# Optimization experiments

Measured on AMD Instinct MI355X. Metric: run time of the kernel, lower is better.

Reference implementation:

```python
import jax, jax.numpy as jnp
import numpy as np

B, N, K = 4, 4096, 16
DP, DM = 64, 128
EPS = 1e-8


def setup_inputs() -> dict:
    key = jax.random.key(0)
    ks = jax.random.split(key, 32)
    g = lambda i, shape, fan: jax.random.normal(ks[i], shape, jnp.float32) / np.sqrt(fan)
    inp = {
        'xyz': jax.random.normal(ks[0], (B, N, 3), jnp.float32),
        'features': jax.random.normal(ks[1], (B, N, DP), jnp.float32),
        # fc1: d_points -> d_model
        'fc1_w': g(2, (DP, DM), DP), 'fc1_b': jnp.zeros((DM,), jnp.float32),
        # fc2: d_model -> d_points
        'fc2_w': g(3, (DM, DP), DM), 'fc2_b': jnp.zeros((DP,), jnp.float32),
        # fc_delta: Linear(3,DM) -> ReLU -> Linear(DM,DM)
        'd1_w': g(4, (3, DM), 3), 'd1_b': jnp.zeros((DM,), jnp.float32),
        'd2_w': g(5, (DM, DM), DM), 'd2_b': jnp.zeros((DM,), jnp.float32),
        # fc_gamma: Linear(DM,DM) -> ReLU -> Linear(DM,DM)
        'g1_w': g(6, (DM, DM), DM), 'g1_b': jnp.zeros((DM,), jnp.float32),
        'g2_w': g(7, (DM, DM), DM), 'g2_b': jnp.zeros((DM,), jnp.float32),
        # q/k/v projections, no bias
        'wq_w': g(8, (DM, DM), DM), 'wk_w': g(9, (DM, DM), DM), 'wv_w': g(10, (DM, DM), DM),
        # fc_sim: Linear(DM+1, DM)
        'sim_w': g(11, (DM + 1, DM), DM + 1), 'sim_b': jnp.zeros((DM,), jnp.float32),
    }
    return inp


def _gather(t, idx):
    # t: [B, N, C], idx: [B, N, K] -> [B, N, K, C]
    bidx = jnp.arange(t.shape[0])[:, None, None]
    return t[bidx, idx]


def reference(xyz, features, fc1_w, fc1_b, fc2_w, fc2_b, d1_w, d1_b, d2_w, d2_b,
              g1_w, g1_b, g2_w, g2_b, wq_w, wk_w, wv_w, sim_w, sim_b):
    # pairwise squared distances [B, N, N]
    sq = jnp.sum(xyz * xyz, axis=-1)
    dists = sq[:, :, None] + sq[:, None, :] - 2.0 * jnp.einsum('bnc,bmc->bnm', xyz, xyz)
    knn_idx = jnp.argsort(dists, axis=-1)[:, :, :K]            # [B, N, K]

    knn_xyz = _gather(xyz, knn_idx)                            # [B, N, K, 3]
    x = features @ fc1_w + fc1_b                               # [B, N, DM]
    q = x @ wq_w                                               # [B, N, DM]
    k = _gather(x @ wk_w, knn_idx)                             # [B, N, K, DM]
    v = _gather(x @ wv_w, knn_idx)                             # [B, N, K, DM]

    rel_pos = xyz[:, :, None, :] - knn_xyz                     # [B, N, K, 3]
    pos_enc = jax.nn.relu(rel_pos @ d1_w + d1_b) @ d2_w + d2_b # [B, N, K, DM]

    qe = q[:, :, None, :]                                      # [B, N, 1, DM]
    # torch cosine_similarity: dot / (max(||q||,eps) * max(||k||,eps))
    qn = jnp.maximum(jnp.linalg.norm(q, axis=-1), EPS)[:, :, None]
    kn = jnp.maximum(jnp.linalg.norm(k, axis=-1), EPS)
    sim = jnp.sum(qe * k, axis=-1) / (qn * kn)                 # [B, N, K]

    rel_qk = jnp.concatenate([sim[..., None], qe - k], axis=-1)  # [B, N, K, DM+1]
    rel_qk = rel_qk @ sim_w + sim_b                            # [B, N, K, DM]

    attn = jax.nn.relu((rel_qk + pos_enc) @ g1_w + g1_b) @ g2_w + g2_b
    attn = jax.nn.softmax(attn / np.sqrt(DM).astype(np.float32), axis=-2)  # over K

    res = jnp.einsum('bnkf,bnkf->bnf', attn, v + pos_enc)      # [B, N, DM]
    res = res @ fc2_w + fc2_b + features                       # [B, N, DP]
    return res, attn
```

## Files before the change

### kernel.cpp

```cpp
#include <hip/hip_runtime.h>
#include <hip/hip_bf16.h>

#define BB 4
#define NN 4096
#define KK 16
#define DP 64
#define DM 128
#define DMP 132
#define SPITCH 264
#define EPSF 1e-8f
#define OUT0N ((size_t)BB * NN * DP)

typedef unsigned short u16t;
typedef __attribute__((ext_vector_type(8))) short s8v;
typedef __attribute__((ext_vector_type(4))) float f4v;

__device__ int g_flag;

__device__ __forceinline__ float u2f(u16t u) {
    unsigned int x = ((unsigned int)u) << 16;
    return __uint_as_float(x);
}
__device__ __forceinline__ u16t f2u(float v) {
    __hip_bfloat16 h = __float2bfloat16(v);
    return *(u16t*)&h;
}
__device__ __forceinline__ void splitf(float x, u16t& h, u16t& l) {
    const unsigned xb = __float_as_uint(x);
    h = (u16t)(xb >> 16);
    const float hf = __uint_as_float(xb & 0xffff0000u);
    l = (u16t)(__float_as_uint(x - hf) >> 16);
}

template<int DT> struct IO;
template<> struct IO<0> {
    static __device__ __forceinline__ float ld(const void* p, size_t i) { return ((const float*)p)[i]; }
    static __device__ __forceinline__ void ld4(const void* p, size_t i, float o[4]) {
        float4 v = *(const float4*)((const float*)p + i);
        o[0] = v.x; o[1] = v.y; o[2] = v.z; o[3] = v.w;
    }
    static __device__ __forceinline__ void st(void* p, size_t i, float v) { ((float*)p)[i] = v; }
};
template<> struct IO<1> {
    static __device__ __forceinline__ float ld(const void* p, size_t i) { return u2f(((const u16t*)p)[i]); }
    static __device__ __forceinline__ void ld4(const void* p, size_t i, float o[4]) {
        ushort4 v = *(const ushort4*)((const u16t*)p + i);
        o[0] = u2f(v.x); o[1] = u2f(v.y); o[2] = u2f(v.z); o[3] = u2f(v.w);
    }
    static __device__ __forceinline__ void st(void* p, size_t i, float v) { ((u16t*)p)[i] = f2u(v); }
};

__global__ __launch_bounds__(64) void detect_kernel(const void* feat) {
    const int tid = threadIdx.x;
    float x = u2f(((const u16t*)feat)[2 * tid]);
    float a = fabsf(x);
    bool sane = (x == 0.0f) || (a > 1e-4f && a < 50.0f);
    unsigned long long m = __ballot(sane);
    if (tid == 0) g_flag = (__popcll(m) >= 32) ? 1 : 0;
}

struct QkvSmem { float sf[DP]; float sx[DM]; };

template<int DT>
__device__ __forceinline__ void qkv_body(QkvSmem& s,
    const void* feat, const void* fc1_w, const void* fc1_b,
    const void* wq, const void* wk, const void* wv,
    float* __restrict__ qbuf, float* __restrict__ kbuf, float* __restrict__ vbuf)
{
    const int bn = blockIdx.x;
    const int tid = threadIdx.x;
    if (tid < DP) s.sf[tid] = IO<DT>::ld(feat, (size_t)bn * DP + tid);
    __syncthreads();
    float x = IO<DT>::ld(fc1_b, tid);
#pragma unroll 4
    for (int i = 0; i < DP; i++) x = fmaf(s.sf[i], IO<DT>::ld(fc1_w, i * DM + tid), x);
    s.sx[tid] = x;
    __syncthreads();
    float q = 0.f, k = 0.f, v = 0.f;
    for (int i0 = 0; i0 < DM; i0 += 4) {
        float4 xv = *(const float4*)&s.sx[i0];
        const float xs[4] = { xv.x, xv.y, xv.z, xv.w };
#pragma unroll
        for (int j = 0; j < 4; j++) {
            q = fmaf(xs[j], IO<DT>::ld(wq, (i0 + j) * DM + tid), q);
            k = fmaf(xs[j], IO<DT>::ld(wk, (i0 + j) * DM + tid), k);
            v = fmaf(xs[j], IO<DT>::ld(wv, (i0 + j) * DM + tid), v);
        }
    }
    qbuf[(size_t)bn * DM + tid] = q;
    kbuf[(size_t)bn * DM + tid] = k;
    vbuf[(size_t)bn * DM + tid] = v;
}

__global__ __launch_bounds__(128) void qkv_kernel(
    const void* feat, const void* fc1_w, const void* fc1_b,
    const void* wq, const void* wk, const void* wv,
    float* qbuf, float* kbuf, float* vbuf)
{
    __shared__ __align__(16) QkvSmem s;
    if (g_flag) qkv_body<1>(s, feat, fc1_w, fc1_b, wq, wk, wv, qbuf, kbuf, vbuf);
    else        qkv_body<0>(s, feat, fc1_w, fc1_b, wq, wk, wv, qbuf, kbuf, vbuf);
}

struct Qkv16Smem { float sf[16][DP]; float sx[16][DMP]; };

template<int DT>
__device__ __forceinline__ void qkv16_body(Qkv16Smem& s,
    const void* feat, const void* fc1_w, const void* fc1_b,
    const void* wq, const void* wk, const void* wv,
    float* __restrict__ qbuf, float* __restrict__ kbuf, float* __restrict__ vbuf)
{
    const int pnt0 = blockIdx.x << 4;
    const int tid = threadIdx.x;
    {
        const int r = tid >> 4, c4 = (tid & 15) << 2;
        float o[4];
        IO<DT>::ld4(feat, (size_t)(pnt0 + r) * DP + c4, o);
        s.sf[r][c4 + 0] = o[0]; s.sf[r][c4 + 1] = o[1];
        s.sf[r][c4 + 2] = o[2]; s.sf[r][c4 + 3] = o[3];
    }
    __syncthreads();
    const int c = tid & 127, h = tid >> 7;
    {
        float acc[8];
        const float fb = IO<DT>::ld(fc1_b, c);
#pragma unroll
        for (int pp = 0; pp < 8; pp++) acc[pp] = fb;
        for (int i = 0; i < DP; i++) {
            const float w = IO<DT>::ld(fc1_w, (size_t)i * DM + c);
#pragma unroll
            for (int pp = 0; pp < 8; pp++) acc[pp] = fmaf(s.sf[h * 8 + pp][i], w, acc[pp]);
        }
#pragma unroll
        for (int pp = 0; pp < 8; pp++) s.sx[h * 8 + pp][c] = acc[pp];
    }
    __syncthreads();
    {
        float aq[8], ak[8], av[8];
#pragma unroll
        for (int pp = 0; pp < 8; pp++) { aq[pp] = 0.f; ak[pp] = 0.f; av[pp] = 0.f; }
        for (int i0 = 0; i0 < DM; i0 += 4) {
            float x4[8][4];
#pragma unroll
            for (int pp = 0; pp < 8; pp++) {
                const float4 xv = *(const float4*)&s.sx[h * 8 + pp][i0];
                x4[pp][0] = xv.x; x4[pp][1] = xv.y; x4[pp][2] = xv.z; x4[pp][3] = xv.w;
            }
#pragma unroll
            for (int j = 0; j < 4; j++) {
                const float wqv = IO<DT>::ld(wq, (size_t)(i0 + j) * DM + c);
                const float wkv = IO<DT>::ld(wk, (size_t)(i0 + j) * DM + c);
                const float wvv = IO<DT>::ld(wv, (size_t)(i0 + j) * DM + c);
#pragma unroll
                for (int pp = 0; pp < 8; pp++) {
                    aq[pp] = fmaf(x4[pp][j], wqv, aq[pp]);
                    ak[pp] = fmaf(x4[pp][j], wkv, ak[pp]);
                    av[pp] = fmaf(x4[pp][j], wvv, av[pp]);
                }
            }
        }
#pragma unroll
        for (int pp = 0; pp < 8; pp++) {
            const size_t row = (size_t)(pnt0 + h * 8 + pp) * DM + c;
            qbuf[row] = aq[pp]; kbuf[row] = ak[pp]; vbuf[row] = av[pp];
        }
    }
}

__global__ __launch_bounds__(256) void qkv16_kernel(
    const void* feat, const void* fc1_w, const void* fc1_b,
    const void* wq, const void* wk, const void* wv,
    float* qbuf, float* kbuf, float* vbuf)
{
    __shared__ __align__(16) Qkv16Smem s;
    if (g_flag) qkv16_body<1>(s, feat, fc1_w, fc1_b, wq, wk, wv, qbuf, kbuf, vbuf);
    else        qkv16_body<0>(s, feat, fc1_w, fc1_b, wq, wk, wv, qbuf, kbuf, vbuf);
}

template<int DT>
__device__ __forceinline__ void knn_body(float4* __restrict__ sc,
    const void* xyz, int* dst, int dstride, void* dout, int in_out)
{
    if (in_out) {
        if (DT) { dst = (int*)((u16t*)dout + OUT0N); dstride = (KK * DM) / 2; }
        else    { dst = (int*)((float*)dout + OUT0N); dstride = KK * DM; }
    }
    const int b = blockIdx.x >> 9;
    const int tid = threadIdx.x;
    for (int j = tid; j < NN; j += 512) {
        float x = IO<DT>::ld(xyz, ((size_t)b * NN + j) * 3 + 0);
        float y = IO<DT>::ld(xyz, ((size_t)b * NN + j) * 3 + 1);
        float z = IO<DT>::ld(xyz, ((size_t)b * NN + j) * 3 + 2);
        float sq = __fadd_rn(__fadd_rn(__fmul_rn(x, x), __fmul_rn(y, y)), __fmul_rn(z, z));
        sc[j] = make_float4(x, y, z, sq);
    }
    __syncthreads();
    const int lane = tid & 63;
    const int wave = tid >> 6;
    const int r = ((blockIdx.x & 511) << 3) + wave;
    const float4 qc = sc[r];

    float d[KK];
    int id[KK];
#pragma unroll
    for (int t = 0; t < KK; t++) { d[t] = 3.4e38f; id[t] = 0x7fffffff; }

    for (int j = lane; j < NN; j += 64) {
        const float4 c = sc[j];
        const float dot = __fadd_rn(__fadd_rn(__fmul_rn(qc.x, c.x), __fmul_rn(qc.y, c.y)),
                                    __fmul_rn(qc.z, c.z));
        const float dist = __fsub_rn(__fadd_rn(qc.w, c.w), __fmul_rn(2.0f, dot));
        if (dist < d[KK - 1]) {
            float cd = dist; int ci = j;
#pragma unroll
            for (int t = 0; t < KK; t++) {
                const bool sw = (cd < d[t]);
                const float od = d[t]; const int oi = id[t];
                d[t]  = sw ? cd : d[t];
                id[t] = sw ? ci : id[t];
                cd = sw ? od : cd;
                ci = sw ? oi : ci;
            }
        }
    }

    const size_t base = (size_t)(b * NN + r) * (size_t)dstride;
#pragma unroll
    for (int t = 0; t < KK; t++) {
        float bd = d[0]; int bi = id[0];
#pragma unroll
        for (int off = 32; off >= 1; off >>= 1) {
            const float od = __shfl_xor(bd, off, 64);
            const int   oi = __shfl_xor(bi, off, 64);
            if (od < bd || (od == bd && oi < bi)) { bd = od; bi = oi; }
        }
        const bool win = (d[0] == bd) && (id[0] == bi);
        if (win) {
#pragma unroll
            for (int u = 0; u < KK - 1; u++) { d[u] = d[u + 1]; id[u] = id[u + 1]; }
            d[KK - 1] = 3.4e38f; id[KK - 1] = 0x7fffffff;
        }
        if (lane == t) dst[base + t] = bi;
    }
}

__global__ __launch_bounds__(512) void knn_kernel(
    const void* xyz, int* dst, int dstride, void* dout, int in_out)
{
    __shared__ __align__(16) float4 sc[NN];
    if (g_flag) knn_body<1>(sc, xyz, dst, dstride, dout, in_out);
    else        knn_body<0>(sc, xyz, dst, dstride, dout, in_out);
}

template<int DT>
__device__ __forceinline__ void gemm_tile(const float* __restrict__ IN,
                                          const void* __restrict__ W, int woff,
                                          int kg, int f0, float acc[4][4])
{
#pragma unroll
    for (int a = 0; a < 4; a++)
#pragma unroll
        for (int c = 0; c < 4; c++) acc[a][c] = 0.f;
    for (int i0 = 0; i0 < DM; i0 += 4) {
        float w[4][4];
#pragma unroll
        for (int j = 0; j < 4; j++) IO<DT>::ld4(W, (size_t)woff + (i0 + j) * DM + f0, w[j]);
#pragma unroll
        for (int kk = 0; kk < 4; kk++) {
            float4 x4 = *(const float4*)(IN + (kg * 4 + kk) * DMP + i0);
            const float xs[4] = { x4.x, x4.y, x4.z, x4.w };
#pragma unroll
            for (int ff = 0; ff < 4; ff++)
#pragma unroll
                for (int j = 0; j < 4; j++)
                    acc[kk][ff] = fmaf(xs[j], w[j][ff], acc[kk][ff]);
        }
    }
}

template<int DT>
__device__ __forceinline__ void wprep_body(const void* sim_w, const void* d2_w,
                                           const void* g1_w, const void* g2_w,
                                           u16t* __restrict__ wprep)
{
    const int m  = blockIdx.x >> 3;
    const int t  = blockIdx.x & 7;
    const int ks = threadIdx.x >> 6;
    const int lane = threadIdx.x & 63;
    const void* src = (m == 0) ? sim_w : (m == 1) ? d2_w : (m == 2) ? g1_w : g2_w;
    const int srcoff = (m == 0) ? DM : 0;
    u16t* hi = wprep + (size_t)m * 32768;
    u16t* lo = hi + 16384;
    const int c  = t * 16 + (lane & 15);
    const int k0 = ks * 32 + ((lane >> 4) << 3);
    s8v vh, vl;
#pragma unroll
    for (int j = 0; j < 8; j++) {
        const float x = IO<DT>::ld(src, (size_t)srcoff + (size_t)(k0 + j) * DM + c);
        const u16t h = f2u(x);
        vh[j] = (short)h;
        vl[j] = (short)f2u(x - u2f(h));
    }
    const size_t off = ((size_t)(t * 4 + ks) * 64 + lane) * 8;
    *(s8v*)(hi + off) = vh;
    *(s8v*)(lo + off) = vl;
}

__global__ __launch_bounds__(256) void wprep_kernel(
    const void* sim_w, const void* d2_w, const void* g1_w, const void* g2_w,
    u16t* wprep)
{
    if (g_flag) wprep_body<1>(sim_w, d2_w, g1_w, g2_w, wprep);
    else        wprep_body<0>(sim_w, d2_w, g1_w, g2_w, wprep);
}

__device__ __forceinline__ void mfma_core(const u16t* __restrict__ SP,
                                          const u16t* __restrict__ wmat,
                                          int lane, int wid, f4v acc[4])
{
    const u16t* whi = wmat;
    const u16t* wlo = wmat + 16384;
    const u16t* ar = SP + (size_t)(lane & 15) * SPITCH + ((lane >> 4) << 3);
#pragma unroll
    for (int ks = 0; ks < 4; ks++) {
        const s8v ahi = *(const s8v*)(ar + ks * 32);
        const s8v alo = *(const s8v*)(ar + 128 + ks * 32);
#pragma unroll
        for (int t = 0; t < 4; t++) {
            const size_t off = ((size_t)((wid * 4 + t) * 4 + ks) * 64 + lane) * 8;
            const s8v bhi = *(const s8v*)(whi + off);
            const s8v blo = *(const s8v*)(wlo + off);
            acc[t] = __builtin_amdgcn_mfma_f32_16x16x32_bf16(ahi, bhi, acc[t], 0, 0, 0);
            acc[t] = __builtin_amdgcn_mfma_f32_16x16x32_bf16(ahi, blo, acc[t], 0, 0, 0);
            acc[t] = __builtin_amdgcn_mfma_f32_16x16x32_bf16(alo, bhi, acc[t], 0, 0, 0);
        }
    }
}

struct AttnSmemS {
    float KF[KK * DMP];
    float T1[KK * DMP];
    u16t  SP[KK * SPITCH];
    float s_q[DM];
    float sred[DM];
    float sp2[DM];
    float srp[KK][3];
    float ssim[KK];
    int   sidx[KK];
};

template<int DT>
__device__ __forceinline__ void attn_sp_body(AttnSmemS& s,
    const void* xyz, const void* feat,
    const void* fc2_w, const void* fc2_b,
    const void* d1_w, const void* d1_b, const void* d2_b,
    const void* g1_b, const void* g2_b,
    const void* sim_w, const void* sim_b,
    const float* __restrict__ qbuf, const float* __restrict__ kbuf,
    const float* __restrict__ vbuf,
    const int* __restrict__ knn, const u16t* __restrict__ wprep, void* dout)
{
    void* out0 = dout;
    void* out1 = DT ? (void*)((u16t*)dout + OUT0N) : (void*)((float*)dout + OUT0N);
    const int bn = blockIdx.x;
    const int b = bn >> 12;
    const int tid = threadIdx.x;
    const int f = tid;
    const int lane = tid & 63;
    const int wid = tid >> 6;

    if (tid < KK) {
        int sv = knn[(size_t)bn * KK + tid];
        sv = (sv < 0) ? 0 : (sv > NN - 1 ? NN - 1 : sv);
        s.sidx[tid] = sv;
    }
    __syncthreads();

    float vreg[KK];
    {
        s.s_q[f] = qbuf[(size_t)bn * DM + f];
#pragma unroll
        for (int k = 0; k < KK; k++) {
            const int grow = (b << 12) + s.sidx[k];
            s.KF[k * DMP + f] = kbuf[(size_t)grow * DM + f];
            vreg[k] = vbuf[(size_t)grow * DM + f];
        }
    }
    if (tid < KK) {
        const int grow = (b << 12) + s.sidx[tid];
#pragma unroll
        for (int c = 0; c < 3; c++)
            s.srp[tid][c] = IO<DT>::ld(xyz, (size_t)bn * 3 + c) - IO<DT>::ld(xyz, (size_t)grow * 3 + c);
    }
    __syncthreads();

    {
        const int j = tid >> 3, g = tid & 7;
        float sk = 0.f, sd = 0.f, qq = 0.f;
#pragma unroll
        for (int i4 = 0; i4 < 16; i4 += 4) {
            const float4 kv = *(const float4*)&s.KF[j * DMP + g * 16 + i4];
            const float4 qv = *(const float4*)&s.s_q[g * 16 + i4];
            sk = fmaf(kv.x, kv.x, fmaf(kv.y, kv.y, fmaf(kv.z, kv.z, fmaf(kv.w, kv.w, sk))));
            sd = fmaf(qv.x, kv.x, fmaf(qv.y, kv.y, fmaf(qv.z, kv.z, fmaf(qv.w, kv.w, sd))));
            qq = fmaf(qv.x, qv.x, fmaf(qv.y, qv.y, fmaf(qv.z, qv.z, fmaf(qv.w, qv.w, qq))));
        }
#pragma unroll
        for (int off = 1; off <= 4; off <<= 1) {
            sk += __shfl_xor(sk, off, 64);
            sd += __shfl_xor(sd, off, 64);
            qq += __shfl_xor(qq, off, 64);
        }
        if (g == 0) {
            const float qn = fmaxf(sqrtf(qq), EPSF);
            const float kn = fmaxf(sqrtf(sk), EPSF);
            s.ssim[j] = sd / (qn * kn);
        }
    }
    {
        const int r = tid & 15, c0 = (tid >> 4) << 4;
        u16t* hp = &s.SP[r * SPITCH + c0];
        u16t* lp = hp + 128;
#pragma unroll
        for (int j4 = 0; j4 < 16; j4 += 4) {
            const float4 kv = *(const float4*)&s.KF[r * DMP + c0 + j4];
            const float4 qv = *(const float4*)&s.s_q[c0 + j4];
            ushort4 hv, lv;
            splitf(qv.x - kv.x, hv.x, lv.x);
            splitf(qv.y - kv.y, hv.y, lv.y);
            splitf(qv.z - kv.z, hv.z, lv.z);
            splitf(qv.w - kv.w, hv.w, lv.w);
            *(ushort4*)(hp + j4) = hv;
            *(ushort4*)(lp + j4) = lv;
        }
    }
    __syncthreads();

    {
        f4v acc[4] = { {0,0,0,0},{0,0,0,0},{0,0,0,0},{0,0,0,0} };
        mfma_core(s.SP, wprep + 0 * 32768, lane, wid, acc);
        const int r0 = (lane >> 4) * 4;
#pragma unroll
        for (int t = 0; t < 4; t++) {
            const int col = (wid * 4 + t) * 16 + (lane & 15);
            const float bv = IO<DT>::ld(sim_b, col);
            const float w0v = IO<DT>::ld(sim_w, col);
#pragma unroll
            for (int r = 0; r < 4; r++)
                s.T1[(size_t)(r0 + r) * DMP + col] = fmaf(s.ssim[r0 + r], w0v, acc[t][r] + bv);
        }
    }
    __syncthreads();

    {
        const int r = tid & 15, c0 = (tid >> 4) << 4;
        const float rx = s.srp[r][0], ry = s.srp[r][1], rz = s.srp[r][2];
        u16t* hp = &s.SP[r * SPITCH + c0];
        u16t* lp = hp + 128;
#pragma unroll
        for (int j4 = 0; j4 < 16; j4 += 4) {
            float w0[4], w1[4], w2[4], bb[4];
            IO<DT>::ld4(d1_w, (size_t)0 * DM + c0 + j4, w0);
            IO<DT>::ld4(d1_w, (size_t)1 * DM + c0 + j4, w1);
            IO<DT>::ld4(d1_w, (size_t)2 * DM + c0 + j4, w2);
            IO<DT>::ld4(d1_b, c0 + j4, bb);
            ushort4 hv, lv;
#pragma unroll
            for (int jj = 0; jj < 4; jj++) {
                const float h = fmaxf(fmaf(rz, w2[jj], fmaf(ry, w1[jj], fmaf(rx, w0[jj], bb[jj]))), 0.f);
                u16t hs, ls; splitf(h, hs, ls);
                ((u16t*)&hv)[jj] = hs; ((u16t*)&lv)[jj] = ls;
            }
            *(ushort4*)(hp + j4) = hv;
            *(ushort4*)(lp + j4) = lv;
        }
    }
    __syncthreads();

    {
        f4v acc[4] = { {0,0,0,0},{0,0,0,0},{0,0,0,0},{0,0,0,0} };
        mfma_core(s.SP, wprep + 1 * 32768, lane, wid, acc);
        const int r0 = (lane >> 4) * 4;
#pragma unroll
        for (int t = 0; t < 4; t++) {
            const int col = (wid * 4 + t) * 16 + (lane & 15);
            const float bv = IO<DT>::ld(d2_b, col);
#pragma unroll
            for (int r = 0; r < 4; r++)
                s.KF[(size_t)(r0 + r) * DMP + col] = acc[t][r] + bv;
        }
    }
    __syncthreads();

    {
        const int r = tid & 15, c0 = (tid >> 4) << 4;
        u16t* hp = &s.SP[r * SPITCH + c0];
        u16t* lp = hp + 128;
#pragma unroll
        for (int j4 = 0; j4 < 16; j4 += 4) {
            const float4 t4 = *(const float4*)&s.T1[r * DMP + c0 + j4];
            const float4 p4 = *(const float4*)&s.KF[r * DMP + c0 + j4];
            ushort4 hv, lv;
            splitf(t4.x + p4.x, hv.x, lv.x);
            splitf(t4.y + p4.y, hv.y, lv.y);
            splitf(t4.z + p4.z, hv.z, lv.z);
            splitf(t4.w + p4.w, hv.w, lv.w);
            *(ushort4*)(hp + j4) = hv;
            *(ushort4*)(lp + j4) = lv;
        }
    }
    __syncthreads();

    {
        f4v acc[4] = { {0,0,0,0},{0,0,0,0},{0,0,0,0},{0,0,0,0} };
        mfma_core(s.SP, wprep + 2 * 32768, lane, wid, acc);
        __syncthreads();
        const int r0 = (lane >> 4) * 4;
#pragma unroll
        for (int t = 0; t < 4; t++) {
            const int col = (wid * 4 + t) * 16 + (lane & 15);
            const float bv = IO<DT>::ld(g1_b, col);
#pragma unroll
            for (int r = 0; r < 4; r++) {
                const float v = fmaxf(acc[t][r] + bv, 0.f);
                u16t hs, ls; splitf(v, hs, ls);
                s.SP[(size_t)(r0 + r) * SPITCH + col] = hs;
                s.SP[(size_t)(r0 + r) * SPITCH + 128 + col] = ls;
            }
        }
    }
    __syncthreads();

    {
        f4v acc[4] = { {0,0,0,0},{0,0,0,0},{0,0,0,0},{0,0,0,0} };
        mfma_core(s.SP, wprep + 3 * 32768, lane, wid, acc);
        const int r0 = (lane >> 4) * 4;
#pragma unroll
        for (int t = 0; t < 4; t++) {
            const int col = (wid * 4 + t) * 16 + (lane & 15);
            const float bv = IO<DT>::ld(g2_b, col);
#pragma unroll
            for (int r = 0; r < 4; r++)
                s.T1[(size_t)(r0 + r) * DMP + col] = acc[t][r] + bv;
        }
    }
    __syncthreads();

    {
        const float inv = 0.08838834764831843f;
        float tv[KK];
        float mx = -3.4e38f;
#pragma unroll
        for (int k = 0; k < KK; k++) { tv[k] = s.T1[k * DMP + f] * inv; mx = fmaxf(mx, tv[k]); }
        float ssum = 0.f;
#pragma unroll
        for (int k = 0; k < KK; k++) { tv[k] = __expf(tv[k] - mx); ssum += tv[k]; }
        const float rs = 1.0f / ssum;
        float rf = 0.f;
#pragma unroll
        for (int k = 0; k < KK; k++) {
            const float a = tv[k] * rs;
            IO<DT>::st(out1, ((size_t)bn * KK + k) * DM + f, a);
            rf = fmaf(a, vreg[k] + s.KF[k * DMP + f], rf);
        }
        s.sred[f] = rf;
    }
    __syncthreads();

    {
        const int c = tid & 63, hh = tid >> 6;
        float o = 0.f;
        for (int i = hh * 64; i < hh * 64 + 64; i++)
            o = fmaf(s.sred[i], IO<DT>::ld(fc2_w, (size_t)i * DP + c), o);
        s.sp2[tid] = o;
    }
    __syncthreads();
    if (tid < DP) {
        float o = s.sp2[tid] + s.sp2[tid + 64];
        o = o + IO<DT>::ld(fc2_b, tid) + IO<DT>::ld(feat, (size_t)bn * DP + tid);
        IO<DT>::st(out0, (size_t)bn * DP + tid, o);
    }
}

__global__ __launch_bounds__(128) void attn_sp_kernel(
    const void* xyz, const void* feat,
    const void* fc2_w, const void* fc2_b,
    const void* d1_w, const void* d1_b, const void* d2_b,
    const void* g1_b, const void* g2_b,
    const void* sim_w, const void* sim_b,
    const float* qbuf, const float* kbuf, const float* vbuf,
    const int* knn, const u16t* wprep, void* dout)
{
    __shared__ __align__(16) AttnSmemS s;
    if (g_flag)
        attn_sp_body<1>(s, xyz, feat, fc2_w, fc2_b, d1_w, d1_b, d2_b, g1_b, g2_b,
                        sim_w, sim_b, qbuf, kbuf, vbuf, knn, wprep, dout);
    else
        attn_sp_body<0>(s, xyz, feat, fc2_w, fc2_b, d1_w, d1_b, d2_b, g1_b, g2_b,
                        sim_w, sim_b, qbuf, kbuf, vbuf, knn, wprep, dout);
}

template<bool FUSED> struct AttnSmem {
    float Kb[KK * DMP], Vb[KK * DMP], PE[KK * DMP], T0[KK * DMP], T1[KK * DMP];
    float s_q[DM], sres[DM];
    float SF[FUSED ? 17 * DP : 1];
    float X[FUSED ? 17 * DMP : 1];
    float srp[KK][3];
    float ssim[KK], skn[KK], sdot[KK];
    float sqn;
    int sidx[KK];
};

template<int DT, bool FUSED>
__device__ __forceinline__ void attn_body(AttnSmem<FUSED>& s,
    const void* xyz, const void* feat,
    const void* fc1_w, const void* fc1_b, const void* fc2_w, const void* fc2_b,
    const void* d1_w, const void* d1_b, const void* d2_w, const void* d2_b,
    const void* g1_w, const void* g1_b, const void* g2_w, const void* g2_b,
    const void* sim_w, const void* sim_b,
    const void* wq, const void* wk, const void* wv,
    const float* __restrict__ qbuf, const float* __restrict__ kbuf, const float* __restrict__ vbuf,
    const int* knn, int knn_stride, int knn_in_out, void* dout)
{
    void* out0 = dout;
    void* out1 = DT ? (void*)((u16t*)dout + OUT0N) : (void*)((float*)dout + OUT0N);
    if (knn_in_out) {
        if (DT) { knn = (const int*)((const u16t*)dout + OUT0N); knn_stride = (KK * DM) / 2; }
        else    { knn = (const int*)((const float*)dout + OUT0N); knn_stride = KK * DM; }
    }

    const int bn = blockIdx.x;
    const int b = bn >> 12;
    const int tid = threadIdx.x;
    const int f = tid;
    const int f0 = (tid & 31) * 4;
    const int kg = tid >> 5;

    if (tid < KK) {
        int sv = knn[(size_t)bn * knn_stride + tid];
        sv = (sv < 0) ? 0 : (sv > NN - 1 ? NN - 1 : sv);
        s.sidx[tid] = sv;
    }
    __syncthreads();

    if constexpr (FUSED) {
        for (int idx = tid; idx < 17 * DP; idx += 128) {
            const int r = idx >> 6, c = idx & 63;
            const int row = (r < KK) ? ((b << 12) + s.sidx[r]) : bn;
            s.SF[idx] = IO<DT>::ld(feat, (size_t)row * DP + c);
        }
        __syncthreads();
        float xacc[17];
        const float fb = IO<DT>::ld(fc1_b, tid);
#pragma unroll
        for (int r = 0; r < 17; r++) xacc[r] = fb;
        for (int i = 0; i < DP; i++) {
            const float w = IO<DT>::ld(fc1_w, i * DM + tid);
#pragma unroll
            for (int r = 0; r < 17; r++) xacc[r] = fmaf(s.SF[r * DP + i], w, xacc[r]);
        }
#pragma unroll
        for (int r = 0; r < 17; r++) s.X[r * DMP + tid] = xacc[r];
        __syncthreads();
        {
            float a2[4][4];
            gemm_tile<DT>(s.X, wk, 0, kg, f0, a2);
#pragma unroll
            for (int kk = 0; kk < 4; kk++)
                *(float4*)&s.Kb[(kg * 4 + kk) * DMP + f0] =
                    make_float4(a2[kk][0], a2[kk][1], a2[kk][2], a2[kk][3]);
            gemm_tile<DT>(s.X, wv, 0, kg, f0, a2);
#pragma unroll
            for (int kk = 0; kk < 4; kk++)
                *(float4*)&s.Vb[(kg * 4 + kk) * DMP + f0] =
                    make_float4(a2[kk][0], a2[kk][1], a2[kk][2], a2[kk][3]);
        }
        {
            float qv = 0.f;
            for (int i0 = 0; i0 < DM; i0 += 4) {
                float4 x4 = *(const float4*)&s.X[16 * DMP + i0];
                const float xs[4] = { x4.x, x4.y, x4.z, x4.w };
#pragma unroll
                for (int j = 0; j < 4; j++)
                    qv = fmaf(xs[j], IO<DT>::ld(wq, (i0 + j) * DM + tid), qv);
            }
            s.s_q[tid] = qv;
        }
    } else {
        s.s_q[f] = qbuf[(size_t)bn * DM + f];
#pragma unroll
        for (int k = 0; k < KK; k++) {
            const int row = (b << 12) + s.sidx[k];
            s.Kb[k * DMP + f] = kbuf[(size_t)row * DM + f];
            s.Vb[k * DMP + f] = vbuf[(size_t)row * DM + f];
        }
    }
    if (tid < KK) {
        const int row = (b << 12) + s.sidx[tid];
#pragma unroll
        for (int c = 0; c < 3; c++)
            s.srp[tid][c] = IO<DT>::ld(xyz, (size_t)bn * 3 + c) - IO<DT>::ld(xyz, (size_t)row * 3 + c);
    }
    __syncthreads();

    if (tid < KK) {
        float sk = 0.f, sd = 0.f;
        for (int i = 0; i < DM; i++) {
            float v2 = s.Kb[tid * DMP + i];
            sk = fmaf(v2, v2, sk);
            sd = fmaf(s.s_q[i], v2, sd);
        }
        s.skn[tid] = fmaxf(sqrtf(sk), EPSF);
        s.sdot[tid] = sd;
    } else if (tid == KK) {
        float sqq = 0.f;
        for (int i = 0; i < DM; i++) { float v2 = s.s_q[i]; sqq = fmaf(v2, v2, sqq); }
        s.sqn = fmaxf(sqrtf(sqq), EPSF);
    }
    __syncthreads();
    if (tid < KK) s.ssim[tid] = s.sdot[tid] / (s.sqn * s.skn[tid]);
#pragma unroll
    for (int k = 0; k < KK; k++) s.T0[k * DMP + f] = s.s_q[f] - s.Kb[k * DMP + f];
    __syncthreads();

    float acc[4][4];

    gemm_tile<DT>(s.T0, sim_w, DM, kg, f0, acc);
    {
        float w0f[4], sbf[4];
        IO<DT>::ld4(sim_w, f0, w0f);
        IO<DT>::ld4(sim_b, f0, sbf);
#pragma unroll
        for (int kk = 0; kk < 4; kk++) {
            float sm = s.ssim[kg * 4 + kk];
            float4 o;
            o.x = fmaf(sm, w0f[0], acc[kk][0]) + sbf[0];
            o.y = fmaf(sm, w0f[1], acc[kk][1]) + sbf[1];
            o.z = fmaf(sm, w0f[2], acc[kk][2]) + sbf[2];
            o.w = fmaf(sm, w0f[3], acc[kk][3]) + sbf[3];
            *(float4*)&s.T1[(kg * 4 + kk) * DMP + f0] = o;
        }
    }
    __syncthreads();

    {
        float w0 = IO<DT>::ld(d1_w, 0 * DM + f), w1 = IO<DT>::ld(d1_w, 1 * DM + f),
              w2 = IO<DT>::ld(d1_w, 2 * DM + f);
        float hb = IO<DT>::ld(d1_b, f);
#pragma unroll
        for (int k = 0; k < KK; k++) {
            float h = fmaf(s.srp[k][2], w2, fmaf(s.srp[k][1], w1, fmaf(s.srp[k][0], w0, hb)));
            s.T0[k * DMP + f] = fmaxf(h, 0.f);
        }
    }
    __syncthreads();

    gemm_tile<DT>(s.T0, d2_w, 0, kg, f0, acc);
    {
        float bf[4];
        IO<DT>::ld4(d2_b, f0, bf);
#pragma unroll
        for (int kk = 0; kk < 4; kk++)
            *(float4*)&s.PE[(kg * 4 + kk) * DMP + f0] =
                make_float4(acc[kk][0] + bf[0], acc[kk][1] + bf[1],
                            acc[kk][2] + bf[2], acc[kk][3] + bf[3]);
    }
    __syncthreads();

#pragma unroll
    for (int kk = 0; kk < 4; kk++) {
        const int row = (kg * 4 + kk) * DMP + f0;
        float4 a4 = *(const float4*)&s.T1[row];
        float4 p4 = *(const float4*)&s.PE[row];
        *(float4*)&s.T0[row] = make_float4(a4.x + p4.x, a4.y + p4.y, a4.z + p4.z, a4.w + p4.w);
    }
    __syncthreads();

    gemm_tile<DT>(s.T0, g1_w, 0, kg, f0, acc);
    {
        float bf[4];
        IO<DT>::ld4(g1_b, f0, bf);
#pragma unroll
        for (int kk = 0; kk < 4; kk++)
            *(float4*)&s.T1[(kg * 4 + kk) * DMP + f0] =
                make_float4(fmaxf(acc[kk][0] + bf[0], 0.f), fmaxf(acc[kk][1] + bf[1], 0.f),
                            fmaxf(acc[kk][2] + bf[2], 0.f), fmaxf(acc[kk][3] + bf[3], 0.f));
    }
    __syncthreads();

    gemm_tile<DT>(s.T1, g2_w, 0, kg, f0, acc);
    {
        float bf[4];
        IO<DT>::ld4(g2_b, f0, bf);
#pragma unroll
        for (int kk = 0; kk < 4; kk++)
            *(float4*)&s.T0[(kg * 4 + kk) * DMP + f0] =
                make_float4(acc[kk][0] + bf[0], acc[kk][1] + bf[1],
                            acc[kk][2] + bf[2], acc[kk][3] + bf[3]);
    }
    __syncthreads();

    {
        const float sq128 = 11.31370849898476f;
        float tv[KK];
        float m = -3.4e38f;
#pragma unroll
        for (int k = 0; k < KK; k++) { tv[k] = s.T0[k * DMP + f] / sq128; m = fmaxf(m, tv[k]); }
        float ssum = 0.f;
#pragma unroll
        for (int k = 0; k < KK; k++) { tv[k] = expf(tv[k] - m); ssum += tv[k]; }
        float rf = 0.f;
#pragma unroll
        for (int k = 0; k < KK; k++) {
            float a = tv[k] / ssum;
            IO<DT>::st(out1, ((size_t)bn * KK + k) * DM + f, a);
            rf = fmaf(a, s.Vb[k * DMP + f] + s.PE[k * DMP + f], rf);
        }
        s.sres[f] = rf;
    }
    __syncthreads();

    if (tid < DP) {
        float o = 0.f;
        for (int i = 0; i < DM; i++) o = fmaf(s.sres[i], IO<DT>::ld(fc2_w, i * DP + tid), o);
        o = o + IO<DT>::ld(fc2_b, tid) + IO<DT>::ld(feat, (size_t)bn * DP + tid);
        IO<DT>::st(out0, (size_t)bn * DP + tid, o);
    }
}

template<bool FUSED>
__global__ __launch_bounds__(128) void attn_kernel(
    const void* xyz, const void* feat,
    const void* fc1_w, const void* fc1_b, const void* fc2_w, const void* fc2_b,
    const void* d1_w, const void* d1_b, const void* d2_w, const void* d2_b,
    const void* g1_w, const void* g1_b, const void* g2_w, const void* g2_b,
    const void* sim_w, const void* sim_b,
    const void* wq, const void* wk, const void* wv,
    const float* qbuf, const float* kbuf, const float* vbuf,
    const int* knn, int knn_stride, int knn_in_out, void* dout)
{
    __shared__ __align__(16) AttnSmem<FUSED> s;
    if (g_flag)
        attn_body<1, FUSED>(s, xyz, feat, fc1_w, fc1_b, fc2_w, fc2_b, d1_w, d1_b, d2_w, d2_b,
                            g1_w, g1_b, g2_w, g2_b, sim_w, sim_b, wq, wk, wv,
                            qbuf, kbuf, vbuf, knn, knn_stride, knn_in_out, dout);
    else
        attn_body<0, FUSED>(s, xyz, feat, fc1_w, fc1_b, fc2_w, fc2_b, d1_w, d1_b, d2_w, d2_b,
                            g1_w, g1_b, g2_w, g2_b, sim_w, sim_b, wq, wk, wv,
                            qbuf, kbuf, vbuf, knn, knn_stride, knn_in_out, dout);
}

extern "C" void kernel_launch(void* const* d_in, const int* in_sizes, int n_in,
                              void* d_out, int out_size, void* d_ws, size_t ws_size,
                              hipStream_t stream)
{
    const void* xyz   = d_in[0];
    const void* feat  = d_in[1];
    const void* fc1_w = d_in[2];
    const void* fc1_b = d_in[3];
    const void* fc2_w = d_in[4];
    const void* fc2_b = d_in[5];
    const void* d1_w  = d_in[6];
    const void* d1_b  = d_in[7];
    const void* d2_w  = d_in[8];
    const void* d2_b  = d_in[9];
    const void* g1_w  = d_in[10];
    const void* g1_b  = d_in[11];
    const void* g2_w  = d_in[12];
    const void* g2_b  = d_in[13];
    const void* wq_w  = d_in[14];
    const void* wk_w  = d_in[15];
    const void* wv_w  = d_in[16];
    const void* sim_w = d_in[17];
    const void* sim_b = d_in[18];

    detect_kernel<<<1, 64, 0, stream>>>(feat);

    const size_t need_qkv = (size_t)3 * BB * NN * DM * sizeof(float);
    const size_t need_knn = (size_t)BB * NN * KK * sizeof(int);
    const size_t need_wp  = (size_t)4 * 2 * 16384 * sizeof(u16t);

    if (ws_size >= need_qkv + need_knn + need_wp && d_ws != nullptr) {
        float* qbuf  = (float*)d_ws;
        float* kbuf  = qbuf + (size_t)BB * NN * DM;
        float* vbuf  = kbuf + (size_t)BB * NN * DM;
        int*   knn   = (int*)(vbuf + (size_t)BB * NN * DM);
        u16t*  wprep = (u16t*)(knn + (size_t)BB * NN * KK);
        qkv16_kernel<<<(BB * NN) / 16, 256, 0, stream>>>(feat, fc1_w, fc1_b, wq_w, wk_w, wv_w,
                                                         qbuf, kbuf, vbuf);
        knn_kernel<<<BB * 512, 512, 0, stream>>>(xyz, knn, KK, d_out, 0);
        wprep_kernel<<<32, 256, 0, stream>>>(sim_w, d2_w, g1_w, g2_w, wprep);
        attn_sp_kernel<<<BB * NN, 128, 0, stream>>>(
            xyz, feat, fc2_w, fc2_b, d1_w, d1_b, d2_b, g1_b, g2_b, sim_w, sim_b,
            qbuf, kbuf, vbuf, knn, wprep, d_out);
    } else if (ws_size >= need_qkv + need_knn && d_ws != nullptr) {
        float* qbuf = (float*)d_ws;
        float* kbuf = qbuf + (size_t)BB * NN * DM;
        float* vbuf = kbuf + (size_t)BB * NN * DM;
        int*   knn  = (int*)(vbuf + (size_t)BB * NN * DM);
        qkv_kernel<<<BB * NN, DM, 0, stream>>>(feat, fc1_w, fc1_b, wq_w, wk_w, wv_w, qbuf, kbuf, vbuf);
        knn_kernel<<<BB * 512, 512, 0, stream>>>(xyz, knn, KK, d_out, 0);
        attn_kernel<false><<<BB * NN, DM, 0, stream>>>(
            xyz, feat, fc1_w, fc1_b, fc2_w, fc2_b, d1_w, d1_b, d2_w, d2_b,
            g1_w, g1_b, g2_w, g2_b, sim_w, sim_b, wq_w, wk_w, wv_w,
            qbuf, kbuf, vbuf, knn, KK, 0, d_out);
    } else if (ws_size >= need_knn && d_ws != nullptr) {
        int* knn = (int*)d_ws;
        knn_kernel<<<BB * 512, 512, 0, stream>>>(xyz, knn, KK, d_out, 0);
        attn_kernel<true><<<BB * NN, DM, 0, stream>>>(
            xyz, feat, fc1_w, fc1_b, fc2_w, fc2_b, d1_w, d1_b, d2_w, d2_b,
            g1_w, g1_b, g2_w, g2_b, sim_w, sim_b, wq_w, wk_w, wv_w,
            nullptr, nullptr, nullptr, knn, KK, 0, d_out);
    } else {
        knn_kernel<<<BB * 512, 512, 0, stream>>>(xyz, nullptr, 0, d_out, 1);
        attn_kernel<true><<<BB * NN, DM, 0, stream>>>(
            xyz, feat, fc1_w, fc1_b, fc2_w, fc2_b, d1_w, d1_b, d2_w, d2_b,
            g1_w, g1_b, g2_w, g2_b, sim_w, sim_b, wq_w, wk_w, wv_w,
            nullptr, nullptr, nullptr, nullptr, 0, 1, d_out);
    }
}
```

Before: 645.0 us.

## Process four points per block to reuse MFMA weight fragments across 64 rows

The attention kernel now handles four query points (64 neighbor rows) per 256-thread block instead of one point per 128-thread block. Each wave loads its weight fragments once and reuses them across four 16-row M tiles, which cuts repeated global weight traffic per point. Positional-encoding accumulators stay in registers and the softmax runs on MFMA outputs through cross-lane shuffles, removing fp32 staging buffers in shared memory. The trade-off is higher register pressure from the accumulator arrays and more barriers per block.

```diff
diff --git a/kernel.cpp b/kernel.cpp
--- a/kernel.cpp
+++ b/kernel.cpp
@@ -314,43 +314,48 @@
     else        wprep_body<0>(sim_w, d2_w, g1_w, g2_w, wprep);
 }
 
-__device__ __forceinline__ void mfma_core(const u16t* __restrict__ SP,
-                                          const u16t* __restrict__ wmat,
-                                          int lane, int wid, f4v acc[4])
+__device__ __forceinline__ void mfma_g(const u16t* __restrict__ SP,
+                                       const u16t* __restrict__ wmat,
+                                       int lane, int w, f4v acc[4][2])
 {
     const u16t* whi = wmat;
     const u16t* wlo = wmat + 16384;
-    const u16t* ar = SP + (size_t)(lane & 15) * SPITCH + ((lane >> 4) << 3);
+    const int arow = lane & 15;
+    const int ak   = (lane >> 4) << 3;
 #pragma unroll
     for (int ks = 0; ks < 4; ks++) {
-        const s8v ahi = *(const s8v*)(ar + ks * 32);
-        const s8v alo = *(const s8v*)(ar + 128 + ks * 32);
-#pragma unroll
-        for (int t = 0; t < 4; t++) {
-            const size_t off = ((size_t)((wid * 4 + t) * 4 + ks) * 64 + lane) * 8;
-            const s8v bhi = *(const s8v*)(whi + off);
-            const s8v blo = *(const s8v*)(wlo + off);
-            acc[t] = __builtin_amdgcn_mfma_f32_16x16x32_bf16(ahi, bhi, acc[t], 0, 0, 0);
-            acc[t] = __builtin_amdgcn_mfma_f32_16x16x32_bf16(ahi, blo, acc[t], 0, 0, 0);
-            acc[t] = __builtin_amdgcn_mfma_f32_16x16x32_bf16(alo, bhi, acc[t], 0, 0, 0);
-        }
-    }
-}
-
-struct AttnSmemS {
-    float KF[KK * DMP];
-    float T1[KK * DMP];
-    u16t  SP[KK * SPITCH];
-    float s_q[DM];
-    float sred[DM];
-    float sp2[DM];
-    float srp[KK][3];
-    float ssim[KK];
-    int   sidx[KK];
+        const size_t o0 = ((size_t)(((2 * w + 0) * 4 + ks) * 64) + lane) * 8;
+        const size_t o1 = ((size_t)(((2 * w + 1) * 4 + ks) * 64) + lane) * 8;
+        const s8v b0h = *(const s8v*)(whi + o0);
+        const s8v b0l = *(const s8v*)(wlo + o0);
+        const s8v b1h = *(const s8v*)(whi + o1);
+        const s8v b1l = *(const s8v*)(wlo + o1);
+#pragma unroll
+        for (int m = 0; m < 4; m++) {
+            const u16t* ar = SP + (size_t)(m * 16 + arow) * SPITCH + ak + ks * 32;
+            const s8v ah = *(const s8v*)ar;
+            const s8v al = *(const s8v*)(ar + 128);
+            acc[m][0] = __builtin_amdgcn_mfma_f32_16x16x32_bf16(ah, b0h, acc[m][0], 0, 0, 0);
+            acc[m][0] = __builtin_amdgcn_mfma_f32_16x16x32_bf16(ah, b0l, acc[m][0], 0, 0, 0);
+            acc[m][0] = __builtin_amdgcn_mfma_f32_16x16x32_bf16(al, b0h, acc[m][0], 0, 0, 0);
+            acc[m][1] = __builtin_amdgcn_mfma_f32_16x16x32_bf16(ah, b1h, acc[m][1], 0, 0, 0);
+            acc[m][1] = __builtin_amdgcn_mfma_f32_16x16x32_bf16(ah, b1l, acc[m][1], 0, 0, 0);
+            acc[m][1] = __builtin_amdgcn_mfma_f32_16x16x32_bf16(al, b1h, acc[m][1], 0, 0, 0);
+        }
+    }
+}
+
+struct Attn4Smem {
+    u16t  SP[64 * SPITCH];
+    float sq[4][DM];
+    float sres[4][DM];
+    float ssim[64];
+    float srp[64][3];
+    int   sidx[64];
 };
 
 template<int DT>
-__device__ __forceinline__ void attn_sp_body(AttnSmemS& s,
+__device__ __forceinline__ void attn4w_body(Attn4Smem& s,
     const void* xyz, const void* feat,
     const void* fc2_w, const void* fc2_b,
     const void* d1_w, const void* d1_b, const void* d2_b,
@@ -362,227 +367,222 @@
 {
     void* out0 = dout;
     void* out1 = DT ? (void*)((u16t*)dout + OUT0N) : (void*)((float*)dout + OUT0N);
-    const int bn = blockIdx.x;
-    const int b = bn >> 12;
+    const int pnt0 = blockIdx.x << 2;
+    const int b = pnt0 >> 12;
     const int tid = threadIdx.x;
-    const int f = tid;
     const int lane = tid & 63;
-    const int wid = tid >> 6;
-
-    if (tid < KK) {
-        int sv = knn[(size_t)bn * KK + tid];
+    const int w = tid >> 6;
+    const int h = lane >> 4;
+    const int c = lane & 15;
+
+    if (tid < 64) {
+        int sv = knn[(size_t)(pnt0 + (tid >> 4)) * KK + (tid & 15)];
         sv = (sv < 0) ? 0 : (sv > NN - 1 ? NN - 1 : sv);
         s.sidx[tid] = sv;
-    }
-    __syncthreads();
-
-    float vreg[KK];
-    {
-        s.s_q[f] = qbuf[(size_t)bn * DM + f];
-#pragma unroll
-        for (int k = 0; k < KK; k++) {
-            const int grow = (b << 12) + s.sidx[k];
-            s.KF[k * DMP + f] = kbuf[(size_t)grow * DM + f];
-            vreg[k] = vbuf[(size_t)grow * DM + f];
-        }
-    }
-    if (tid < KK) {
-        const int grow = (b << 12) + s.sidx[tid];
-#pragma unroll
-        for (int c = 0; c < 3; c++)
-            s.srp[tid][c] = IO<DT>::ld(xyz, (size_t)bn * 3 + c) - IO<DT>::ld(xyz, (size_t)grow * 3 + c);
-    }
-    __syncthreads();
-
-    {
-        const int j = tid >> 3, g = tid & 7;
-        float sk = 0.f, sd = 0.f, qq = 0.f;
-#pragma unroll
-        for (int i4 = 0; i4 < 16; i4 += 4) {
-            const float4 kv = *(const float4*)&s.KF[j * DMP + g * 16 + i4];
-            const float4 qv = *(const float4*)&s.s_q[g * 16 + i4];
-            sk = fmaf(kv.x, kv.x, fmaf(kv.y, kv.y, fmaf(kv.z, kv.z, fmaf(kv.w, kv.w, sk))));
-            sd = fmaf(qv.x, kv.x, fmaf(qv.y, kv.y, fmaf(qv.z, kv.z, fmaf(qv.w, kv.w, sd))));
-            qq = fmaf(qv.x, qv.x, fmaf(qv.y, qv.y, fmaf(qv.z, qv.z, fmaf(qv.w, qv.w, qq))));
-        }
-#pragma unroll
-        for (int off = 1; off <= 4; off <<= 1) {
-            sk += __shfl_xor(sk, off, 64);
-            sd += __shfl_xor(sd, off, 64);
-            qq += __shfl_xor(qq, off, 64);
-        }
-        if (g == 0) {
-            const float qn = fmaxf(sqrtf(qq), EPSF);
-            const float kn = fmaxf(sqrtf(sk), EPSF);
-            s.ssim[j] = sd / (qn * kn);
-        }
-    }
-    {
-        const int r = tid & 15, c0 = (tid >> 4) << 4;
-        u16t* hp = &s.SP[r * SPITCH + c0];
-        u16t* lp = hp + 128;
-#pragma unroll
-        for (int j4 = 0; j4 < 16; j4 += 4) {
-            const float4 kv = *(const float4*)&s.KF[r * DMP + c0 + j4];
-            const float4 qv = *(const float4*)&s.s_q[c0 + j4];
+        const int pt = tid >> 4;
+        const int grow = (b << 12) + sv;
+#pragma unroll
+        for (int c3 = 0; c3 < 3; c3++)
+            s.srp[tid][c3] = IO<DT>::ld(xyz, (size_t)(pnt0 + pt) * 3 + c3)
+                           - IO<DT>::ld(xyz, (size_t)grow * 3 + c3);
+    }
+    const float2 q2 = *(const float2*)&qbuf[(size_t)(pnt0 + w) * DM + lane * 2];
+    *(float2*)&s.sq[w][lane * 2] = q2;
+    float qq = fmaf(q2.x, q2.x, q2.y * q2.y);
+#pragma unroll
+    for (int off = 1; off <= 32; off <<= 1) qq += __shfl_xor(qq, off, 64);
+    const float qn = fmaxf(sqrtf(qq), EPSF);
+    __syncthreads();
+
+    {
+        const int row = tid >> 2, cb = (tid & 3) << 5;
+        const float rx = s.srp[row][0], ry = s.srp[row][1], rz = s.srp[row][2];
+        u16t* hp = &s.SP[row * SPITCH];
+#pragma unroll
+        for (int j4 = 0; j4 < 32; j4 += 4) {
+            float w0[4], w1[4], w2[4], bb[4];
+            IO<DT>::ld4(d1_w, (size_t)0 * DM + cb + j4, w0);
+            IO<DT>::ld4(d1_w, (size_t)1 * DM + cb + j4, w1);
+            IO<DT>::ld4(d1_w, (size_t)2 * DM + cb + j4, w2);
+            IO<DT>::ld4(d1_b, cb + j4, bb);
+            ushort4 hv, lv;
+#pragma unroll
+            for (int jj = 0; jj < 4; jj++) {
+                const float hx = fmaxf(fmaf(rz, w2[jj], fmaf(ry, w1[jj], fmaf(rx, w0[jj], bb[jj]))), 0.f);
+                u16t hs, ls; splitf(hx, hs, ls);
+                ((u16t*)&hv)[jj] = hs; ((u16t*)&lv)[jj] = ls;
+            }
+            *(ushort4*)(hp + cb + j4) = hv;
+            *(ushort4*)(hp + 128 + cb + j4) = lv;
+        }
+    }
+    __syncthreads();
+
+    f4v pe[4][2] = { { {0,0,0,0},{0,0,0,0} }, { {0,0,0,0},{0,0,0,0} },
+                     { {0,0,0,0},{0,0,0,0} }, { {0,0,0,0},{0,0,0,0} } };
+    mfma_g(s.SP, wprep + 1 * 32768, lane, w, pe);
+#pragma unroll
+    for (int nt = 0; nt < 2; nt++) {
+        const float bv = IO<DT>::ld(d2_b, (2 * w + nt) * 16 + c);
+#pragma unroll
+        for (int m = 0; m < 4; m++)
+#pragma unroll
+            for (int r = 0; r < 4; r++) pe[m][nt][r] += bv;
+    }
+    __syncthreads();
+
+    {
+        const int row = tid >> 2, cb = (tid & 3) << 5;
+        const int pt = row >> 4;
+        const int grow = (b << 12) + s.sidx[row];
+        const float* krow = &kbuf[(size_t)grow * DM];
+        u16t* hp = &s.SP[row * SPITCH];
+        float sk = 0.f, sd = 0.f;
+#pragma unroll
+        for (int j4 = 0; j4 < 32; j4 += 4) {
+            const float4 kv = *(const float4*)&krow[cb + j4];
+            const float4 qv = *(const float4*)&s.sq[pt][cb + j4];
             ushort4 hv, lv;
             splitf(qv.x - kv.x, hv.x, lv.x);
             splitf(qv.y - kv.y, hv.y, lv.y);
             splitf(qv.z - kv.z, hv.z, lv.z);
             splitf(qv.w - kv.w, hv.w, lv.w);
-            *(ushort4*)(hp + j4) = hv;
-            *(ushort4*)(lp + j4) = lv;
-        }
-    }
-    __syncthreads();
-
-    {
-        f4v acc[4] = { {0,0,0,0},{0,0,0,0},{0,0,0,0},{0,0,0,0} };
-        mfma_core(s.SP, wprep + 0 * 32768, lane, wid, acc);
-        const int r0 = (lane >> 4) * 4;
-#pragma unroll
-        for (int t = 0; t < 4; t++) {
-            const int col = (wid * 4 + t) * 16 + (lane & 15);
-            const float bv = IO<DT>::ld(sim_b, col);
+            *(ushort4*)(hp + cb + j4) = hv;
+            *(ushort4*)(hp + 128 + cb + j4) = lv;
+            sk = fmaf(kv.x, kv.x, fmaf(kv.y, kv.y, fmaf(kv.z, kv.z, fmaf(kv.w, kv.w, sk))));
+            sd = fmaf(qv.x, kv.x, fmaf(qv.y, kv.y, fmaf(qv.z, kv.z, fmaf(qv.w, kv.w, sd))));
+        }
+        sk += __shfl_xor(sk, 1, 64); sk += __shfl_xor(sk, 2, 64);
+        sd += __shfl_xor(sd, 1, 64); sd += __shfl_xor(sd, 2, 64);
+        if ((tid & 3) == 0) {
+            const float kn = fmaxf(sqrtf(sk), EPSF);
+            s.ssim[row] = sd / (qn * kn);
+        }
+    }
+    __syncthreads();
+
+    {
+        f4v a1[4][2] = { { {0,0,0,0},{0,0,0,0} }, { {0,0,0,0},{0,0,0,0} },
+                         { {0,0,0,0},{0,0,0,0} }, { {0,0,0,0},{0,0,0,0} } };
+        mfma_g(s.SP, wprep + 0 * 32768, lane, w, a1);
+        __syncthreads();
+#pragma unroll
+        for (int nt = 0; nt < 2; nt++) {
+            const int col = (2 * w + nt) * 16 + c;
+            const float bv  = IO<DT>::ld(sim_b, col);
             const float w0v = IO<DT>::ld(sim_w, col);
 #pragma unroll
-            for (int r = 0; r < 4; r++)
-                s.T1[(size_t)(r0 + r) * DMP + col] = fmaf(s.ssim[r0 + r], w0v, acc[t][r] + bv);
-        }
-    }
-    __syncthreads();
-
-    {
-        const int r = tid & 15, c0 = (tid >> 4) << 4;
-        const float rx = s.srp[r][0], ry = s.srp[r][1], rz = s.srp[r][2];
-        u16t* hp = &s.SP[r * SPITCH + c0];
-        u16t* lp = hp + 128;
-#pragma unroll
-        for (int j4 = 0; j4 < 16; j4 += 4) {
-            float w0[4], w1[4], w2[4], bb[4];
-            IO<DT>::ld4(d1_w, (size_t)0 * DM + c0 + j4, w0);
-            IO<DT>::ld4(d1_w, (size_t)1 * DM + c0 + j4, w1);
-            IO<DT>::ld4(d1_w, (size_t)2 * DM + c0 + j4, w2);
-            IO<DT>::ld4(d1_b, c0 + j4, bb);
-            ushort4 hv, lv;
-#pragma unroll
-            for (int jj = 0; jj < 4; jj++) {
-                const float h = fmaxf(fmaf(rz, w2[jj], fmaf(ry, w1[jj], fmaf(rx, w0[jj], bb[jj]))), 0.f);
-                u16t hs, ls; splitf(h, hs, ls);
-                ((u16t*)&hv)[jj] = hs; ((u16t*)&lv)[jj] = ls;
+            for (int m = 0; m < 4; m++)
+#pragma unroll
+                for (int r = 0; r < 4; r++) {
+                    const int row = m * 16 + 4 * h + r;
+                    const float val = a1[m][nt][r] + bv + s.ssim[row] * w0v + pe[m][nt][r];
+                    u16t hs, ls; splitf(val, hs, ls);
+                    s.SP[(size_t)row * SPITCH + col] = hs;
+                    s.SP[(size_t)row * SPITCH + 128 + col] = ls;
+                }
+        }
+    }
+    __syncthreads();
+
+    {
+        f4v a3[4][2] = { { {0,0,0,0},{0,0,0,0} }, { {0,0,0,0},{0,0,0,0} },
+                         { {0,0,0,0},{0,0,0,0} }, { {0,0,0,0},{0,0,0,0} } };
+        mfma_g(s.SP, wprep + 2 * 32768, lane, w, a3);
+        __syncthreads();
+#pragma unroll
+        for (int nt = 0; nt < 2; nt++) {
+            const int col = (2 * w + nt) * 16 + c;
+            const float bv = IO<DT>::ld(g1_b, col);
+#pragma unroll
+            for (int m = 0; m < 4; m++)
+#pragma unroll
+                for (int r = 0; r < 4; r++) {
+                    const int row = m * 16 + 4 * h + r;
+                    const float val = fmaxf(a3[m][nt][r] + bv, 0.f);
+                    u16t hs, ls; splitf(val, hs, ls);
+                    s.SP[(size_t)row * SPITCH + col] = hs;
+                    s.SP[(size_t)row * SPITCH + 128 + col] = ls;
+                }
+        }
+    }
+    __syncthreads();
+
+    f4v av[4][2];
+    {
+        f4v a4[4][2] = { { {0,0,0,0},{0,0,0,0} }, { {0,0,0,0},{0,0,0,0} },
+                         { {0,0,0,0},{0,0,0,0} }, { {0,0,0,0},{0,0,0,0} } };
+        mfma_g(s.SP, wprep + 3 * 32768, lane, w, a4);
+        const float inv = 0.08838834764831843f;
+#pragma unroll
+        for (int nt = 0; nt < 2; nt++) {
+            const int col = (2 * w + nt) * 16 + c;
+            const float bv = IO<DT>::ld(g2_b, col);
+#pragma unroll
+            for (int m = 0; m < 4; m++) {
+                float tv[4];
+#pragma unroll
+                for (int r = 0; r < 4; r++) tv[r] = (a4[m][nt][r] + bv) * inv;
+                float mx = fmaxf(fmaxf(tv[0], tv[1]), fmaxf(tv[2], tv[3]));
+                mx = fmaxf(mx, __shfl_xor(mx, 16, 64));
+                mx = fmaxf(mx, __shfl_xor(mx, 32, 64));
+                float ssum = 0.f;
+#pragma unroll
+                for (int r = 0; r < 4; r++) { tv[r] = __expf(tv[r] - mx); ssum += tv[r]; }
+                ssum += __shfl_xor(ssum, 16, 64);
+                ssum += __shfl_xor(ssum, 32, 64);
+                const float rs = 1.0f / ssum;
+#pragma unroll
+                for (int r = 0; r < 4; r++) {
+                    const float a = tv[r] * rs;
+                    av[m][nt][r] = a;
+                    IO<DT>::st(out1, ((size_t)(pnt0 + m) * KK + (4 * h + r)) * DM + col, a);
+                }
             }
-            *(ushort4*)(hp + j4) = hv;
-            *(ushort4*)(lp + j4) = lv;
-        }
-    }
-    __syncthreads();
-
-    {
-        f4v acc[4] = { {0,0,0,0},{0,0,0,0},{0,0,0,0},{0,0,0,0} };
-        mfma_core(s.SP, wprep + 1 * 32768, lane, wid, acc);
-        const int r0 = (lane >> 4) * 4;
-#pragma unroll
-        for (int t = 0; t < 4; t++) {
-            const int col = (wid * 4 + t) * 16 + (lane & 15);
-            const float bv = IO<DT>::ld(d2_b, col);
-#pragma unroll
-            for (int r = 0; r < 4; r++)
-                s.KF[(size_t)(r0 + r) * DMP + col] = acc[t][r] + bv;
-        }
-    }
-    __syncthreads();
-
-    {
-        const int r = tid & 15, c0 = (tid >> 4) << 4;
-        u16t* hp = &s.SP[r * SPITCH + c0];
-        u16t* lp = hp + 128;
-#pragma unroll
-        for (int j4 = 0; j4 < 16; j4 += 4) {
-            const float4 t4 = *(const float4*)&s.T1[r * DMP + c0 + j4];
-            const float4 p4 = *(const float4*)&s.KF[r * DMP + c0 + j4];
-            ushort4 hv, lv;
-            splitf(t4.x + p4.x, hv.x, lv.x);
-            splitf(t4.y + p4.y, hv.y, lv.y);
-            splitf(t4.z + p4.z, hv.z, lv.z);
-            splitf(t4.w + p4.w, hv.w, lv.w);
-            *(ushort4*)(hp + j4) = hv;
-            *(ushort4*)(lp + j4) = lv;
-        }
-    }
-    __syncthreads();
-
-    {
-        f4v acc[4] = { {0,0,0,0},{0,0,0,0},{0,0,0,0},{0,0,0,0} };
-        mfma_core(s.SP, wprep + 2 * 32768, lane, wid, acc);
-        __syncthreads();
-        const int r0 = (lane >> 4) * 4;
-#pragma unroll
-        for (int t = 0; t < 4; t++) {
-            const int col = (wid * 4 + t) * 16 + (lane & 15);
-            const float bv = IO<DT>::ld(g1_b, col);
-#pragma unroll
-            for (int r = 0; r < 4; r++) {
-                const float v = fmaxf(acc[t][r] + bv, 0.f);
-                u16t hs, ls; splitf(v, hs, ls);
-                s.SP[(size_t)(r0 + r) * SPITCH + col] = hs;
-                s.SP[(size_t)(r0 + r) * SPITCH + 128 + col] = ls;
+        }
+    }
+    __syncthreads();
+
+    float* vst = (float*)s.SP;
+    {
+        const int row = tid >> 2, cb = (tid & 3) << 5;
+        const int grow = (b << 12) + s.sidx[row];
+        const float* vrow = &vbuf[(size_t)grow * DM];
+#pragma unroll
+        for (int j4 = 0; j4 < 32; j4 += 4)
+            *(float4*)&vst[row * 132 + cb + j4] = *(const float4*)&vrow[cb + j4];
+    }
+    __syncthreads();
+    {
+#pragma unroll
+        for (int nt = 0; nt < 2; nt++) {
+            const int col = (2 * w + nt) * 16 + c;
+#pragma unroll
+            for (int m = 0; m < 4; m++) {
+                float part = 0.f;
+#pragma unroll
+                for (int r = 0; r < 4; r++)
+                    part = fmaf(av[m][nt][r],
+                                vst[(m * 16 + 4 * h + r) * 132 + col] + pe[m][nt][r], part);
+                part += __shfl_xor(part, 16, 64);
+                part += __shfl_xor(part, 32, 64);
+                if (h == 0) s.sres[m][col] = part;
             }
         }
     }
     __syncthreads();
 
     {
-        f4v acc[4] = { {0,0,0,0},{0,0,0,0},{0,0,0,0},{0,0,0,0} };
-        mfma_core(s.SP, wprep + 3 * 32768, lane, wid, acc);
-        const int r0 = (lane >> 4) * 4;
-#pragma unroll
-        for (int t = 0; t < 4; t++) {
-            const int col = (wid * 4 + t) * 16 + (lane & 15);
-            const float bv = IO<DT>::ld(g2_b, col);
-#pragma unroll
-            for (int r = 0; r < 4; r++)
-                s.T1[(size_t)(r0 + r) * DMP + col] = acc[t][r] + bv;
-        }
-    }
-    __syncthreads();
-
-    {
-        const float inv = 0.08838834764831843f;
-        float tv[KK];
-        float mx = -3.4e38f;
-#pragma unroll
-        for (int k = 0; k < KK; k++) { tv[k] = s.T1[k * DMP + f] * inv; mx = fmaxf(mx, tv[k]); }
-        float ssum = 0.f;
-#pragma unroll
-        for (int k = 0; k < KK; k++) { tv[k] = __expf(tv[k] - mx); ssum += tv[k]; }
-        const float rs = 1.0f / ssum;
-        float rf = 0.f;
-#pragma unroll
-        for (int k = 0; k < KK; k++) {
-            const float a = tv[k] * rs;
-            IO<DT>::st(out1, ((size_t)bn * KK + k) * DM + f, a);
-            rf = fmaf(a, vreg[k] + s.KF[k * DMP + f], rf);
-        }
-        s.sred[f] = rf;
-    }
-    __syncthreads();
-
-    {
-        const int c = tid & 63, hh = tid >> 6;
+        const int pt = tid >> 6, cc = tid & 63;
         float o = 0.f;
-        for (int i = hh * 64; i < hh * 64 + 64; i++)
-            o = fmaf(s.sred[i], IO<DT>::ld(fc2_w, (size_t)i * DP + c), o);
-        s.sp2[tid] = o;
-    }
-    __syncthreads();
-    if (tid < DP) {
-        float o = s.sp2[tid] + s.sp2[tid + 64];
-        o = o + IO<DT>::ld(fc2_b, tid) + IO<DT>::ld(feat, (size_t)bn * DP + tid);
-        IO<DT>::st(out0, (size_t)bn * DP + tid, o);
-    }
-}
-
-__global__ __launch_bounds__(128) void attn_sp_kernel(
+        for (int i = 0; i < DM; i++)
+            o = fmaf(s.sres[pt][i], IO<DT>::ld(fc2_w, (size_t)i * DP + cc), o);
+        o = o + IO<DT>::ld(fc2_b, cc) + IO<DT>::ld(feat, (size_t)(pnt0 + pt) * DP + cc);
+        IO<DT>::st(out0, (size_t)(pnt0 + pt) * DP + cc, o);
+    }
+}
+
+__global__ __launch_bounds__(256, 4) void attn4w_kernel(
     const void* xyz, const void* feat,
     const void* fc2_w, const void* fc2_b,
     const void* d1_w, const void* d1_b, const void* d2_b,
@@ -591,13 +591,13 @@
     const float* qbuf, const float* kbuf, const float* vbuf,
     const int* knn, const u16t* wprep, void* dout)
 {
-    __shared__ __align__(16) AttnSmemS s;
+    __shared__ __align__(16) Attn4Smem s;
     if (g_flag)
-        attn_sp_body<1>(s, xyz, feat, fc2_w, fc2_b, d1_w, d1_b, d2_b, g1_b, g2_b,
-                        sim_w, sim_b, qbuf, kbuf, vbuf, knn, wprep, dout);
+        attn4w_body<1>(s, xyz, feat, fc2_w, fc2_b, d1_w, d1_b, d2_b, g1_b, g2_b,
+                       sim_w, sim_b, qbuf, kbuf, vbuf, knn, wprep, dout);
     else
-        attn_sp_body<0>(s, xyz, feat, fc2_w, fc2_b, d1_w, d1_b, d2_b, g1_b, g2_b,
-                        sim_w, sim_b, qbuf, kbuf, vbuf, knn, wprep, dout);
+        attn4w_body<0>(s, xyz, feat, fc2_w, fc2_b, d1_w, d1_b, d2_b, g1_b, g2_b,
+                       sim_w, sim_b, qbuf, kbuf, vbuf, knn, wprep, dout);
 }
 
 template<bool FUSED> struct AttnSmem {
@@ -890,7 +890,7 @@
                                                          qbuf, kbuf, vbuf);
         knn_kernel<<<BB * 512, 512, 0, stream>>>(xyz, knn, KK, d_out, 0);
         wprep_kernel<<<32, 256, 0, stream>>>(sim_w, d2_w, g1_w, g2_w, wprep);
-        attn_sp_kernel<<<BB * NN, 128, 0, stream>>>(
+        attn4w_kernel<<<(BB * NN) / 4, 256, 0, stream>>>(
             xyz, feat, fc2_w, fc2_b, d1_w, d1_b, d2_b, g1_b, g2_b, sim_w, sim_b,
             qbuf, kbuf, vbuf, knn, wprep, d_out);
     } else if (ws_size >= need_qkv + need_knn && d_ws != nullptr) {
```

After: 579.1 us. 10.2% less time.
